# Optimization experiments

Hardware: AMD Instinct MI355X
Metric: run time of the kernel (lower is better)

The kernel has to match this reference:

```python
import jax, jax.numpy as jnp
import numpy as np

EMBED = 1024
HEADS = 16
HEAD_DIM = EMBED // HEADS


def setup_inputs() -> dict:
    key = jax.random.key(0)
    ks = jax.random.split(key, 8)
    N, S = 4, 2048
    scale = 1.0 / np.sqrt(HEAD_DIM)
    return {
        "values": jax.random.normal(ks[0], (N, S, EMBED), jnp.float32),
        "keys": jax.random.normal(ks[1], (N, S, EMBED), jnp.float32),
        "query": jax.random.normal(ks[2], (N, S, EMBED), jnp.float32),
        "Wv": jax.random.normal(ks[3], (HEAD_DIM, HEAD_DIM), jnp.float32) * scale,
        "Wk": jax.random.normal(ks[4], (HEAD_DIM, HEAD_DIM), jnp.float32) * scale,
        "Wq": jax.random.normal(ks[5], (HEAD_DIM, HEAD_DIM), jnp.float32) * scale,
        "Wo": jax.random.normal(ks[6], (EMBED, EMBED), jnp.float32) / np.sqrt(EMBED),
        "bo": jax.random.normal(ks[7], (EMBED,), jnp.float32) * 0.01,
    }


def reference(values, keys, query, Wv, Wk, Wq, Wo, bo):
    N = query.shape[0]
    # reshape to [N, S, H, D]
    v = values.reshape(N, -1, HEADS, HEAD_DIM)
    k = keys.reshape(N, -1, HEADS, HEAD_DIM)
    q = query.reshape(N, -1, HEADS, HEAD_DIM)
    # per-head linear projections (torch Linear: x @ W.T)
    v = jnp.einsum("nshd,ed->nshe", v, Wv)
    k = jnp.einsum("nshd,ed->nshe", k, Wk)
    q = jnp.einsum("nshd,ed->nshe", q, Wq)
    # full attention matrix [N, H, Q, K]; note scale uses embed_size**0.5 as in source
    energy = jnp.einsum("nqhd,nkhd->nhqk", q, k)
    attn = jax.nn.softmax(energy / jnp.sqrt(jnp.asarray(EMBED, energy.dtype)), axis=3)
    out = jnp.einsum("nhql,nlhd->nqhd", attn, v).reshape(N, -1, EMBED)
    return out @ Wo.T + bo
```

## Files before the change

### kernel.cpp

```cpp
#include <hip/hip_runtime.h>
#include <hip/hip_bf16.h>

#define EMBED 1024
#define HEADS 16
#define HD    64
#define NB    4
#define SEQ   2048

typedef __bf16 bf16x2 __attribute__((ext_vector_type(2)));
typedef __bf16 bf16x8 __attribute__((ext_vector_type(8)));
typedef float  f32x4  __attribute__((ext_vector_type(4)));
typedef float  f32x16 __attribute__((ext_vector_type(16)));
typedef unsigned uint2v __attribute__((ext_vector_type(2)));

__device__ __forceinline__ unsigned short f2bf(float f) {
    union { float f; unsigned u; } v; v.f = f;
    unsigned r = v.u + 0x7fffu + ((v.u >> 16) & 1u);
    return (unsigned short)(r >> 16);
}
__device__ __forceinline__ unsigned pack2(float a, float b) {
#if __has_builtin(__builtin_amdgcn_cvt_pk_bf16_f32)
    union { bf16x2 v; unsigned u; } c;
    c.v = __builtin_amdgcn_cvt_pk_bf16_f32(a, b);
    return c.u;
#else
    return (unsigned)f2bf(a) | ((unsigned)f2bf(b) << 16);
#endif
}

__global__ __launch_bounds__(256) void cvt_kernel(const float* __restrict__ src,
                                                  unsigned* __restrict__ dst) {
    int i = blockIdx.x * 256 + threadIdx.x;
    float4 v = ((const float4*)src)[i];
    uint2 o;
    o.x = pack2(v.x, v.y);
    o.y = pack2(v.z, v.w);
    ((uint2*)dst)[i] = o;
}

__global__ __launch_bounds__(256) void proj_kernel(
    const float* __restrict__ xq, const float* __restrict__ xk, const float* __restrict__ xv,
    const float* __restrict__ Wq, const float* __restrict__ Wk, const float* __restrict__ Wv,
    unsigned short* __restrict__ Qp, unsigned short* __restrict__ Kp, unsigned short* __restrict__ Vt)
{
    __shared__ __align__(16) unsigned short Wl[64 * 72];
    __shared__ __align__(16) unsigned short Xl[256 * 72];

    int bx = blockIdx.x;
    int p  = bx >> 9;
    int r  = bx & 511;
    int st = r & 7, h = (r >> 3) & 15, n = r >> 7;
    int s0 = st * 256;

    const float* x = (p == 0) ? xq : (p == 1) ? xk : xv;
    const float* W = (p == 0) ? Wq : (p == 1) ? Wk : Wv;
    const float sc = (p == 0) ? 0.045084220027780106f : 1.0f;

    int tid = threadIdx.x;

    for (int i = 0; i < 4; ++i) {
        int idx = tid + i * 256;
        int row = idx >> 4, c4 = idx & 15;
        float4 wv = ((const float4*)W)[row * 16 + c4];
        uint2 pw;
        pw.x = pack2(wv.x, wv.y);
        pw.y = pack2(wv.z, wv.w);
        *(uint2*)&Wl[row * 72 + c4 * 4] = pw;
    }
    const float* xbase = x + (size_t)(n * SEQ + s0) * EMBED + h * HD;
    for (int i = 0; i < 16; ++i) {
        int idx = tid + i * 256;
        int row = idx >> 4, c4 = idx & 15;
        float4 v = *(const float4*)(xbase + (size_t)row * EMBED + c4 * 4);
        uint2 px;
        px.x = pack2(v.x, v.y);
        px.y = pack2(v.z, v.w);
        *(uint2*)&Xl[row * 72 + c4 * 4] = px;
    }
    __syncthreads();

    int w = tid >> 6, lane = tid & 63, ln = lane & 15, qd = lane >> 4;

    bf16x8 a[4][2], b[4][2];
#pragma unroll
    for (int mt = 0; mt < 4; ++mt)
#pragma unroll
        for (int kt = 0; kt < 2; ++kt)
            a[mt][kt] = *(const bf16x8*)&Xl[(w * 64 + mt * 16 + ln) * 72 + kt * 32 + qd * 8];
#pragma unroll
    for (int i = 0; i < 4; ++i)
#pragma unroll
        for (int kt = 0; kt < 2; ++kt)
            b[i][kt] = *(const bf16x8*)&Wl[(i * 16 + ln) * 72 + kt * 32 + qd * 8];

    f32x4 acc[4][4];
    const f32x4 fz = {0.f, 0.f, 0.f, 0.f};
#pragma unroll
    for (int i = 0; i < 4; ++i)
#pragma unroll
        for (int j = 0; j < 4; ++j) acc[i][j] = fz;

    if (p < 2) {
#pragma unroll
        for (int i = 0; i < 4; ++i)
#pragma unroll
            for (int j = 0; j < 4; ++j) {
                acc[i][j] = __builtin_amdgcn_mfma_f32_16x16x32_bf16(b[i][0], a[j][0], acc[i][j], 0, 0, 0);
                acc[i][j] = __builtin_amdgcn_mfma_f32_16x16x32_bf16(b[i][1], a[j][1], acc[i][j], 0, 0, 0);
            }
#pragma unroll
        for (int i = 0; i < 4; ++i)
#pragma unroll
            for (int j = 0; j < 4; ++j) {
                uint2 pk;
                pk.x = pack2(acc[i][j][0] * sc, acc[i][j][1] * sc);
                pk.y = pack2(acc[i][j][2] * sc, acc[i][j][3] * sc);
                *(uint2*)&Xl[(w * 64 + j * 16 + ln) * 72 + i * 16 + qd * 4] = pk;
            }
        __syncthreads();
        unsigned short* outp = (p == 0 ? Qp : Kp) + (size_t)(n * HEADS + h) * SEQ * HD + (size_t)s0 * HD;
        for (int i = 0; i < 8; ++i) {
            int idx = tid + i * 256;
            int row = idx >> 3, ch = idx & 7;
            *(uint4*)(outp + (size_t)row * HD + ch * 8) = *(const uint4*)&Xl[row * 72 + ch * 8];
        }
    } else {
#pragma unroll
        for (int mt = 0; mt < 4; ++mt)
#pragma unroll
            for (int i = 0; i < 4; ++i) {
                acc[mt][i] = __builtin_amdgcn_mfma_f32_16x16x32_bf16(a[mt][0], b[i][0], acc[mt][i], 0, 0, 0);
                acc[mt][i] = __builtin_amdgcn_mfma_f32_16x16x32_bf16(a[mt][1], b[i][1], acc[mt][i], 0, 0, 0);
            }
        __syncthreads();
#pragma unroll
        for (int mt = 0; mt < 4; ++mt)
#pragma unroll
            for (int i = 0; i < 4; ++i) {
                uint2 pk;
                pk.x = pack2(acc[mt][i][0], acc[mt][i][1]);
                pk.y = pack2(acc[mt][i][2], acc[mt][i][3]);
                *(uint2*)&Xl[(i * 16 + ln) * 264 + w * 64 + mt * 16 + qd * 4] = pk;
            }
        __syncthreads();
        unsigned short* outp = Vt + (size_t)(n * HEADS + h) * HD * SEQ + s0;
        for (int i = 0; i < 8; ++i) {
            int idx = tid + i * 256;
            int row = idx >> 5, ch = idx & 31;
            *(uint4*)(outp + (size_t)row * SEQ + ch * 8) = *(const uint4*)&Xl[row * 264 + ch * 8];
        }
    }
}

__global__ __launch_bounds__(512, 4) void attn_kernel(
    const unsigned short* __restrict__ Qp, const unsigned short* __restrict__ Kp,
    const unsigned short* __restrict__ Vt, unsigned short* __restrict__ Xattn)
{
    __shared__ __align__(16) unsigned short SMEM[18432];
    unsigned short* Kl = SMEM;
    unsigned short* Vl = SMEM + 9216;

    int bx = blockIdx.x;
    int head = bx >> 3, qt = bx & 7;
    int n = head >> 4, h16 = head & 15;
    int q0 = qt * 256;

    int tid = threadIdx.x;
    int w = tid >> 6, lane = tid & 63;
    int qc = lane & 31, hh = lane >> 5;

    const unsigned short* Qb = Qp + (size_t)head * SEQ * HD;
    const unsigned short* Kb = Kp + (size_t)head * SEQ * HD;
    const unsigned short* Vb = Vt + (size_t)head * HD * SEQ;

    bf16x8 qb[4];
    {
        int qrow = q0 + w * 32 + qc;
#pragma unroll
        for (int kk = 0; kk < 4; ++kk)
            qb[kk] = *(const bf16x8*)(Qb + (size_t)qrow * HD + kk * 16 + hh * 8);
    }

    f32x16 ot0, ot1;
#pragma unroll
    for (int i = 0; i < 16; ++i) { ot0[i] = 0.f; ot1[i] = 0.f; }
    float ls[4] = {0.f, 0.f, 0.f, 0.f};

    int srow = tid >> 3, sch = tid & 7;

    uint4 rK, rV;
    rK = *(const uint4*)(Kb + (size_t)srow * HD + sch * 8);
    rV = *(const uint4*)(Vb + (size_t)srow * SEQ + 0 + sch * 8);
    *(uint4*)&Kl[srow * 72 + sch * 8] = rK;
    *(uint4*)&Vl[srow * 72 + sch * 8] = rV;
    rK = *(const uint4*)(Kb + (size_t)(64 + srow) * HD + sch * 8);
    rV = *(const uint4*)(Vb + (size_t)srow * SEQ + 64 + sch * 8);

    for (int kc = 0; kc < SEQ; kc += 64) {
        int cur = (kc >> 6) & 1, nxt = cur ^ 1;
        int curo = cur * 4608;
        __syncthreads();

        if (kc + 64 < SEQ) {
            *(uint4*)&Kl[nxt * 4608 + srow * 72 + sch * 8] = rK;
            *(uint4*)&Vl[nxt * 4608 + srow * 72 + sch * 8] = rV;
            int kn = kc + 128 <= SEQ - 64 ? kc + 128 : SEQ - 64;
            rK = *(const uint4*)(Kb + (size_t)(kn + srow) * HD + sch * 8);
            rV = *(const uint4*)(Vb + (size_t)srow * SEQ + kn + sch * 8);
        }

        unsigned pk[2][8];
#pragma unroll
        for (int kt = 0; kt < 2; ++kt) {
            f32x16 c;
#pragma unroll
            for (int i = 0; i < 16; ++i) c[i] = 0.f;
#pragma unroll
            for (int kk = 0; kk < 4; ++kk) {
                bf16x8 ka = *(const bf16x8*)&Kl[curo + (kt * 32 + qc) * 72 + kk * 16 + hh * 8];
                c = __builtin_amdgcn_mfma_f32_32x32x16_bf16(ka, qb[kk], c, 0, 0, 0);
            }
#pragma unroll
            for (int i = 0; i < 8; ++i) {
                float p0 = __builtin_amdgcn_exp2f(c[2 * i]);
                float p1 = __builtin_amdgcn_exp2f(c[2 * i + 1]);
                ls[i & 3] += p0 + p1;
                pk[kt][i] = pack2(p0, p1);
            }
        }

#pragma unroll
        for (int g = 0; g < 4; ++g) {
            const unsigned* P = pk[g >> 1];
            int base = (g & 1) * 4;
            union { unsigned u[4]; bf16x8 v; } bb;
#if __has_builtin(__builtin_amdgcn_permlane32_swap)
            uint2v r  = __builtin_amdgcn_permlane32_swap(P[base + 0], P[base + 2], false, false);
            uint2v rr = __builtin_amdgcn_permlane32_swap(P[base + 1], P[base + 3], false, false);
            bb.u[0] = r.x;
            bb.u[1] = rr.x;
            bb.u[2] = r.y;
            bb.u[3] = rr.y;
#else
            unsigned s0 = hh ? P[base + 0] : P[base + 2];
            unsigned s1 = hh ? P[base + 1] : P[base + 3];
            unsigned r0 = (unsigned)__shfl_xor((int)s0, 32);
            unsigned r1 = (unsigned)__shfl_xor((int)s1, 32);
            bb.u[0] = hh ? r0 : P[base + 0];
            bb.u[1] = hh ? r1 : P[base + 1];
            bb.u[2] = hh ? P[base + 2] : r0;
            bb.u[3] = hh ? P[base + 3] : r1;
#endif
            bf16x8 va0 = *(const bf16x8*)&Vl[curo + qc * 72 + g * 16 + hh * 8];
            bf16x8 va1 = *(const bf16x8*)&Vl[curo + (32 + qc) * 72 + g * 16 + hh * 8];
            ot0 = __builtin_amdgcn_mfma_f32_32x32x16_bf16(va0, bb.v, ot0, 0, 0, 0);
            ot1 = __builtin_amdgcn_mfma_f32_32x32x16_bf16(va1, bb.v, ot1, 0, 0, 0);
        }
    }

    float lsum = (ls[0] + ls[1]) + (ls[2] + ls[3]);
    lsum += __shfl_xor(lsum, 32);
    float inv = 1.0f / lsum;

    __syncthreads();
    int qlocal = w * 32 + qc;
#pragma unroll
    for (int dt = 0; dt < 2; ++dt) {
        const f32x16& o = dt ? ot1 : ot0;
#pragma unroll
        for (int g = 0; g < 4; ++g) {
            uint2 p;
            p.x = pack2(o[4 * g + 0] * inv, o[4 * g + 1] * inv);
            p.y = pack2(o[4 * g + 2] * inv, o[4 * g + 3] * inv);
            *(uint2*)&SMEM[qlocal * 72 + dt * 32 + g * 8 + hh * 4] = p;
        }
    }
    __syncthreads();
    unsigned short* ob = Xattn + (size_t)(n * SEQ + q0) * EMBED + h16 * HD;
#pragma unroll
    for (int i = 0; i < 4; ++i) {
        int idx = tid + i * 512;
        int row = idx >> 3, ch = idx & 7;
        *(uint4*)(ob + (size_t)row * EMBED + ch * 8) = *(const uint4*)&SMEM[row * 72 + ch * 8];
    }
}

__global__ __launch_bounds__(256, 4) void outproj_kernel(
    const unsigned short* __restrict__ X, const unsigned short* __restrict__ Wb,
    const float* __restrict__ bo, float* __restrict__ out)
{
    __shared__ __align__(16) unsigned short Al[64 * 72];
    __shared__ __align__(16) unsigned short Bl[128 * 72];

    int bx = blockIdx.x;
    int cm = bx >> 3, cn = bx & 7;
    int m0 = cm * 64, c0 = cn * 128;
    int tid = threadIdx.x;
    int w = tid >> 6, lane = tid & 63, ln = lane & 15, qd = lane >> 4;
    int chw = w * 32;

    f32x4 acc[4][2];
    const f32x4 fz = {0.f, 0.f, 0.f, 0.f};
#pragma unroll
    for (int mt = 0; mt < 4; ++mt)
#pragma unroll
        for (int nt = 0; nt < 2; ++nt) acc[mt][nt] = fz;

    for (int k0 = 0; k0 < EMBED; k0 += 64) {
        {
            int row = tid >> 3, ch = tid & 7;
            if (tid < 512) {
            }
#pragma unroll
            for (int i = 0; i < 2; ++i) {
                int idx = tid + i * 256;
                int r2 = idx >> 3, c2 = idx & 7;
                uint4 av = *(const uint4*)(X + (size_t)(m0 + r2) * EMBED + k0 + c2 * 8);
                *(uint4*)&Al[r2 * 72 + c2 * 8] = av;
            }
#pragma unroll
            for (int i = 0; i < 4; ++i) {
                int idx = tid + i * 256;
                int r2 = idx >> 3, c2 = idx & 7;
                uint4 bv = *(const uint4*)(Wb + (size_t)(c0 + r2) * EMBED + k0 + c2 * 8);
                *(uint4*)&Bl[r2 * 72 + c2 * 8] = bv;
            }
            (void)row; (void)ch;
        }
        __syncthreads();
        bf16x8 af[4][2], bf_[2][2];
#pragma unroll
        for (int mt = 0; mt < 4; ++mt)
#pragma unroll
            for (int kt = 0; kt < 2; ++kt)
                af[mt][kt] = *(const bf16x8*)&Al[(mt * 16 + ln) * 72 + kt * 32 + qd * 8];
#pragma unroll
        for (int nt = 0; nt < 2; ++nt)
#pragma unroll
            for (int kt = 0; kt < 2; ++kt)
                bf_[nt][kt] = *(const bf16x8*)&Bl[(chw + nt * 16 + ln) * 72 + kt * 32 + qd * 8];
#pragma unroll
        for (int mt = 0; mt < 4; ++mt)
#pragma unroll
            for (int nt = 0; nt < 2; ++nt) {
                acc[mt][nt] = __builtin_amdgcn_mfma_f32_16x16x32_bf16(af[mt][0], bf_[nt][0], acc[mt][nt], 0, 0, 0);
                acc[mt][nt] = __builtin_amdgcn_mfma_f32_16x16x32_bf16(af[mt][1], bf_[nt][1], acc[mt][nt], 0, 0, 0);
            }
        __syncthreads();
    }

#pragma unroll
    for (int nt = 0; nt < 2; ++nt) {
        int col = c0 + chw + nt * 16 + ln;
        float bias = bo[col];
#pragma unroll
        for (int mt = 0; mt < 4; ++mt) {
            int row = m0 + mt * 16 + qd * 4;
#pragma unroll
            for (int rg = 0; rg < 4; ++rg)
                out[(size_t)(row + rg) * EMBED + col] = acc[mt][nt][rg] + bias;
        }
    }
}

extern "C" void kernel_launch(void* const* d_in, const int* in_sizes, int n_in,
                              void* d_out, int out_size, void* d_ws, size_t ws_size,
                              hipStream_t stream) {
    const float* values = (const float*)d_in[0];
    const float* keys   = (const float*)d_in[1];
    const float* query  = (const float*)d_in[2];
    const float* Wv     = (const float*)d_in[3];
    const float* Wk     = (const float*)d_in[4];
    const float* Wq     = (const float*)d_in[5];
    const float* Wo     = (const float*)d_in[6];
    const float* bo     = (const float*)d_in[7];
    float* out = (float*)d_out;

    unsigned short* ws = (unsigned short*)d_ws;
    const size_t HSZ = (size_t)NB * HEADS * SEQ * HD;
    unsigned short* Qp = ws;
    unsigned short* Kp = Qp + HSZ;
    unsigned short* Vt = Kp + HSZ;
    unsigned short* Xa = Vt + HSZ;
    unsigned short* Wb = Xa + HSZ;

    cvt_kernel<<<1024, 256, 0, stream>>>(Wo, (unsigned*)Wb);
    proj_kernel<<<1536, 256, 0, stream>>>(query, keys, values, Wq, Wk, Wv, Qp, Kp, Vt);
    attn_kernel<<<512, 512, 0, stream>>>(Qp, Kp, Vt, Xa);
    outproj_kernel<<<1024, 256, 0, stream>>>(Xa, Wb, bo, out);
}
```

Baseline: 271.8 us.

## Split attention into 128-query blocks, swizzle block order, add MFMA priority hints

The attention kernel moves from 512-thread blocks covering 256 queries to 256-thread blocks covering 128 queries, doubling the grid to 1024 blocks. Each thread now stages two K/V rows per tile. Blocks are remapped so consecutive block IDs spread across heads (likely for XCD/L2 locality), and s_setprio raises wave priority around the MFMA sections. The smaller blocks aim for better occupancy and load balance, but each K/V tile is now loaded twice as often per query.

After: 334.0 us. +22.9%, slower.

```diff
diff --git a/kernel.cpp b/kernel.cpp
--- a/kernel.cpp
+++ b/kernel.cpp
@@ -152,7 +152,7 @@
     }
 }
 
-__global__ __launch_bounds__(512, 4) void attn_kernel(
+__global__ __launch_bounds__(256, 4) void attn_kernel(
     const unsigned short* __restrict__ Qp, const unsigned short* __restrict__ Kp,
     const unsigned short* __restrict__ Vt, unsigned short* __restrict__ Xattn)
 {
@@ -160,10 +160,11 @@
     unsigned short* Kl = SMEM;
     unsigned short* Vl = SMEM + 9216;
 
-    int bx = blockIdx.x;
-    int head = bx >> 3, qt = bx & 7;
+    int pb = blockIdx.x;
+    int bx = (pb & 7) * 128 + (pb >> 3);
+    int head = bx >> 4, qt = bx & 15;
     int n = head >> 4, h16 = head & 15;
-    int q0 = qt * 256;
+    int q0 = qt * 128;
 
     int tid = threadIdx.x;
     int w = tid >> 6, lane = tid & 63;
@@ -188,13 +189,21 @@
 
     int srow = tid >> 3, sch = tid & 7;
 
-    uint4 rK, rV;
-    rK = *(const uint4*)(Kb + (size_t)srow * HD + sch * 8);
-    rV = *(const uint4*)(Vb + (size_t)srow * SEQ + 0 + sch * 8);
-    *(uint4*)&Kl[srow * 72 + sch * 8] = rK;
-    *(uint4*)&Vl[srow * 72 + sch * 8] = rV;
-    rK = *(const uint4*)(Kb + (size_t)(64 + srow) * HD + sch * 8);
-    rV = *(const uint4*)(Vb + (size_t)srow * SEQ + 64 + sch * 8);
+    uint4 rK[2], rV[2];
+#pragma unroll
+    for (int i = 0; i < 2; ++i) {
+        int rr = srow + i * 32;
+        rK[i] = *(const uint4*)(Kb + (size_t)rr * HD + sch * 8);
+        rV[i] = *(const uint4*)(Vb + (size_t)rr * SEQ + 0 + sch * 8);
+        *(uint4*)&Kl[rr * 72 + sch * 8] = rK[i];
+        *(uint4*)&Vl[rr * 72 + sch * 8] = rV[i];
+    }
+#pragma unroll
+    for (int i = 0; i < 2; ++i) {
+        int rr = srow + i * 32;
+        rK[i] = *(const uint4*)(Kb + (size_t)(64 + rr) * HD + sch * 8);
+        rV[i] = *(const uint4*)(Vb + (size_t)rr * SEQ + 64 + sch * 8);
+    }
 
     for (int kc = 0; kc < SEQ; kc += 64) {
         int cur = (kc >> 6) & 1, nxt = cur ^ 1;
@@ -202,11 +211,19 @@
         __syncthreads();
 
         if (kc + 64 < SEQ) {
-            *(uint4*)&Kl[nxt * 4608 + srow * 72 + sch * 8] = rK;
-            *(uint4*)&Vl[nxt * 4608 + srow * 72 + sch * 8] = rV;
+#pragma unroll
+            for (int i = 0; i < 2; ++i) {
+                int rr = srow + i * 32;
+                *(uint4*)&Kl[nxt * 4608 + rr * 72 + sch * 8] = rK[i];
+                *(uint4*)&Vl[nxt * 4608 + rr * 72 + sch * 8] = rV[i];
+            }
             int kn = kc + 128 <= SEQ - 64 ? kc + 128 : SEQ - 64;
-            rK = *(const uint4*)(Kb + (size_t)(kn + srow) * HD + sch * 8);
-            rV = *(const uint4*)(Vb + (size_t)srow * SEQ + kn + sch * 8);
+#pragma unroll
+            for (int i = 0; i < 2; ++i) {
+                int rr = srow + i * 32;
+                rK[i] = *(const uint4*)(Kb + (size_t)(kn + rr) * HD + sch * 8);
+                rV[i] = *(const uint4*)(Vb + (size_t)rr * SEQ + kn + sch * 8);
+            }
         }
 
         unsigned pk[2][8];
@@ -215,11 +232,13 @@
             f32x16 c;
 #pragma unroll
             for (int i = 0; i < 16; ++i) c[i] = 0.f;
+            __builtin_amdgcn_s_setprio(1);
 #pragma unroll
             for (int kk = 0; kk < 4; ++kk) {
                 bf16x8 ka = *(const bf16x8*)&Kl[curo + (kt * 32 + qc) * 72 + kk * 16 + hh * 8];
                 c = __builtin_amdgcn_mfma_f32_32x32x16_bf16(ka, qb[kk], c, 0, 0, 0);
             }
+            __builtin_amdgcn_s_setprio(0);
 #pragma unroll
             for (int i = 0; i < 8; ++i) {
                 float p0 = __builtin_amdgcn_exp2f(c[2 * i]);
@@ -229,6 +248,7 @@
             }
         }
 
+        __builtin_amdgcn_s_setprio(1);
 #pragma unroll
         for (int g = 0; g < 4; ++g) {
             const unsigned* P = pk[g >> 1];
@@ -256,6 +276,7 @@
             ot0 = __builtin_amdgcn_mfma_f32_32x32x16_bf16(va0, bb.v, ot0, 0, 0, 0);
             ot1 = __builtin_amdgcn_mfma_f32_32x32x16_bf16(va1, bb.v, ot1, 0, 0, 0);
         }
+        __builtin_amdgcn_s_setprio(0);
     }
 
     float lsum = (ls[0] + ls[1]) + (ls[2] + ls[3]);
@@ -279,7 +300,7 @@
     unsigned short* ob = Xattn + (size_t)(n * SEQ + q0) * EMBED + h16 * HD;
 #pragma unroll
     for (int i = 0; i < 4; ++i) {
-        int idx = tid + i * 512;
+        int idx = tid + i * 256;
         int row = idx >> 3, ch = idx & 7;
         *(uint4*)(ob + (size_t)row * EMBED + ch * 8) = *(const uint4*)&SMEM[row * 72 + ch * 8];
     }
@@ -308,9 +329,6 @@
 
     for (int k0 = 0; k0 < EMBED; k0 += 64) {
         {
-            int row = tid >> 3, ch = tid & 7;
-            if (tid < 512) {
-            }
 #pragma unroll
             for (int i = 0; i < 2; ++i) {
                 int idx = tid + i * 256;
@@ -325,7 +343,6 @@
                 uint4 bv = *(const uint4*)(Wb + (size_t)(c0 + r2) * EMBED + k0 + c2 * 8);
                 *(uint4*)&Bl[r2 * 72 + c2 * 8] = bv;
             }
-            (void)row; (void)ch;
         }
         __syncthreads();
         bf16x8 af[4][2], bf_[2][2];
@@ -386,6 +403,6 @@
 
     cvt_kernel<<<1024, 256, 0, stream>>>(Wo, (unsigned*)Wb);
     proj_kernel<<<1536, 256, 0, stream>>>(query, keys, values, Wq, Wk, Wv, Qp, Kp, Vt);
-    attn_kernel<<<512, 512, 0, stream>>>(Qp, Kp, Vt, Xa);
+    attn_kernel<<<1024, 256, 0, stream>>>(Qp, Kp, Vt, Xa);
     outproj_kernel<<<1024, 256, 0, stream>>>(Xa, Wb, bo, out);
 }
```

## Fuse all four stages into one persistent kernel with grid barriers

Applied to the files above, without the earlier changes.

Merges the Wo conversion, QKV projection, attention and output projection into a single 512-block persistent kernel. The stages are separated by a software grid barrier, an atomic counter plus a generation flag stored in the last two words of the output buffer and zeroed by a memset. This removes the launch gaps and tail effects between separate kernels. The projection now runs three smaller tiles per block, and the output projection moves to 128x128 tiles on 512 blocks. The design relies on all blocks being co-resident, and the barrier words are later overwritten by output writes. A spin timeout can silently break synchronisation.

Measured after the change: 451.6 us. +66.1%, slower.

```diff
diff --git a/kernel.cpp b/kernel.cpp
--- a/kernel.cpp
+++ b/kernel.cpp
@@ -6,6 +6,7 @@
 #define HD    64
 #define NB    4
 #define SEQ   2048
+#define NBLK  512
 
 typedef __bf16 bf16x2 __attribute__((ext_vector_type(2)));
 typedef __bf16 bf16x8 __attribute__((ext_vector_type(8)));
@@ -28,337 +29,352 @@
 #endif
 }
 
-__global__ __launch_bounds__(256) void cvt_kernel(const float* __restrict__ src,
-                                                  unsigned* __restrict__ dst) {
-    int i = blockIdx.x * 256 + threadIdx.x;
-    float4 v = ((const float4*)src)[i];
-    uint2 o;
-    o.x = pack2(v.x, v.y);
-    o.y = pack2(v.z, v.w);
-    ((uint2*)dst)[i] = o;
-}
-
-__global__ __launch_bounds__(256) void proj_kernel(
-    const float* __restrict__ xq, const float* __restrict__ xk, const float* __restrict__ xv,
-    const float* __restrict__ Wq, const float* __restrict__ Wk, const float* __restrict__ Wv,
-    unsigned short* __restrict__ Qp, unsigned short* __restrict__ Kp, unsigned short* __restrict__ Vt)
-{
-    __shared__ __align__(16) unsigned short Wl[64 * 72];
-    __shared__ __align__(16) unsigned short Xl[256 * 72];
-
-    int bx = blockIdx.x;
-    int p  = bx >> 9;
-    int r  = bx & 511;
-    int st = r & 7, h = (r >> 3) & 15, n = r >> 7;
-    int s0 = st * 256;
-
-    const float* x = (p == 0) ? xq : (p == 1) ? xk : xv;
-    const float* W = (p == 0) ? Wq : (p == 1) ? Wk : Wv;
-    const float sc = (p == 0) ? 0.045084220027780106f : 1.0f;
-
-    int tid = threadIdx.x;
-
-    for (int i = 0; i < 4; ++i) {
-        int idx = tid + i * 256;
-        int row = idx >> 4, c4 = idx & 15;
-        float4 wv = ((const float4*)W)[row * 16 + c4];
-        uint2 pw;
-        pw.x = pack2(wv.x, wv.y);
-        pw.y = pack2(wv.z, wv.w);
-        *(uint2*)&Wl[row * 72 + c4 * 4] = pw;
-    }
-    const float* xbase = x + (size_t)(n * SEQ + s0) * EMBED + h * HD;
-    for (int i = 0; i < 16; ++i) {
-        int idx = tid + i * 256;
-        int row = idx >> 4, c4 = idx & 15;
-        float4 v = *(const float4*)(xbase + (size_t)row * EMBED + c4 * 4);
-        uint2 px;
-        px.x = pack2(v.x, v.y);
-        px.y = pack2(v.z, v.w);
-        *(uint2*)&Xl[row * 72 + c4 * 4] = px;
+__device__ __forceinline__ void grid_barrier(unsigned* cnt, unsigned* gen, unsigned phase) {
+    __syncthreads();
+    if (threadIdx.x == 0) {
+        __threadfence();
+        unsigned prev = atomicAdd(cnt, 1u);
+        if (prev == NBLK * (phase + 1) - 1) {
+            __hip_atomic_store(gen, phase + 1, __ATOMIC_RELEASE, __HIP_MEMORY_SCOPE_AGENT);
+        } else {
+            long long spins = 0;
+            while (__hip_atomic_load(gen, __ATOMIC_ACQUIRE, __HIP_MEMORY_SCOPE_AGENT) < phase + 1) {
+                __builtin_amdgcn_s_sleep(2);
+                if (++spins > (1LL << 22)) break;
+            }
+        }
+        __threadfence();
     }
     __syncthreads();
-
-    int w = tid >> 6, lane = tid & 63, ln = lane & 15, qd = lane >> 4;
-
-    bf16x8 a[4][2], b[4][2];
-#pragma unroll
-    for (int mt = 0; mt < 4; ++mt)
-#pragma unroll
-        for (int kt = 0; kt < 2; ++kt)
-            a[mt][kt] = *(const bf16x8*)&Xl[(w * 64 + mt * 16 + ln) * 72 + kt * 32 + qd * 8];
-#pragma unroll
-    for (int i = 0; i < 4; ++i)
-#pragma unroll
-        for (int kt = 0; kt < 2; ++kt)
-            b[i][kt] = *(const bf16x8*)&Wl[(i * 16 + ln) * 72 + kt * 32 + qd * 8];
-
-    f32x4 acc[4][4];
-    const f32x4 fz = {0.f, 0.f, 0.f, 0.f};
-#pragma unroll
-    for (int i = 0; i < 4; ++i)
-#pragma unroll
-        for (int j = 0; j < 4; ++j) acc[i][j] = fz;
-
-    if (p < 2) {
-#pragma unroll
-        for (int i = 0; i < 4; ++i)
-#pragma unroll
-            for (int j = 0; j < 4; ++j) {
-                acc[i][j] = __builtin_amdgcn_mfma_f32_16x16x32_bf16(b[i][0], a[j][0], acc[i][j], 0, 0, 0);
-                acc[i][j] = __builtin_amdgcn_mfma_f32_16x16x32_bf16(b[i][1], a[j][1], acc[i][j], 0, 0, 0);
-            }
-#pragma unroll
-        for (int i = 0; i < 4; ++i)
-#pragma unroll
-            for (int j = 0; j < 4; ++j) {
-                uint2 pk;
-                pk.x = pack2(acc[i][j][0] * sc, acc[i][j][1] * sc);
-                pk.y = pack2(acc[i][j][2] * sc, acc[i][j][3] * sc);
-                *(uint2*)&Xl[(w * 64 + j * 16 + ln) * 72 + i * 16 + qd * 4] = pk;
-            }
+}
+
+__global__ __launch_bounds__(512, 4) void mega_kernel(
+    const float* __restrict__ values, const float* __restrict__ keys,
+    const float* __restrict__ query,
+    const float* __restrict__ Wv, const float* __restrict__ Wk,
+    const float* __restrict__ Wq,
+    const float* __restrict__ Wo, const float* __restrict__ bo,
+    unsigned short* __restrict__ Qp, unsigned short* __restrict__ Kp,
+    unsigned short* __restrict__ Vt, unsigned short* __restrict__ Xa,
+    unsigned short* __restrict__ Wb, float* __restrict__ out)
+{
+    __shared__ __align__(16) unsigned short SMEM[23040];
+    unsigned* bar = (unsigned*)(out + (size_t)NB * SEQ * EMBED - 2);
+
+    int bx = blockIdx.x;
+    int tid = threadIdx.x;
+
+    {
+        int i = bx * 512 + tid;
+        float4 v = ((const float4*)Wo)[i];
+        uint2 o;
+        o.x = pack2(v.x, v.y);
+        o.y = pack2(v.z, v.w);
+        ((uint2*)Wb)[i] = o;
+    }
+
+    {
+        unsigned short* Wl = SMEM;
+        unsigned short* Xl = SMEM + 4608;
+        int w = tid >> 6, lane = tid & 63, ln = lane & 15, qd = lane >> 4;
+
+        for (int t = 0; t < 3; ++t) {
+            int id = bx * 3 + t;
+            int p = id >> 9, r = id & 511;
+            int st = r & 7, h = (r >> 3) & 15, n = r >> 7;
+            int s0 = st * 256;
+            const float* x = (p == 0) ? query : (p == 1) ? keys : values;
+            const float* W = (p == 0) ? Wq : (p == 1) ? Wk : Wv;
+            const float sc = (p == 0) ? 0.045084220027780106f : 1.0f;
+
+            __syncthreads();
+#pragma unroll
+            for (int i2 = 0; i2 < 2; ++i2) {
+                int idx = tid + i2 * 512;
+                int row = idx >> 4, c4 = idx & 15;
+                float4 wv = ((const float4*)W)[row * 16 + c4];
+                uint2 pw;
+                pw.x = pack2(wv.x, wv.y);
+                pw.y = pack2(wv.z, wv.w);
+                *(uint2*)&Wl[row * 72 + c4 * 4] = pw;
+            }
+            const float* xbase = x + (size_t)(n * SEQ + s0) * EMBED + h * HD;
+#pragma unroll
+            for (int i2 = 0; i2 < 8; ++i2) {
+                int idx = tid + i2 * 512;
+                int row = idx >> 4, c4 = idx & 15;
+                float4 v = *(const float4*)(xbase + (size_t)row * EMBED + c4 * 4);
+                uint2 px;
+                px.x = pack2(v.x, v.y);
+                px.y = pack2(v.z, v.w);
+                *(uint2*)&Xl[row * 72 + c4 * 4] = px;
+            }
+            __syncthreads();
+
+            bf16x8 a[2][2], b[4][2];
+#pragma unroll
+            for (int mt = 0; mt < 2; ++mt)
+#pragma unroll
+                for (int kt = 0; kt < 2; ++kt)
+                    a[mt][kt] = *(const bf16x8*)&Xl[(w * 32 + mt * 16 + ln) * 72 + kt * 32 + qd * 8];
+#pragma unroll
+            for (int i2 = 0; i2 < 4; ++i2)
+#pragma unroll
+                for (int kt = 0; kt < 2; ++kt)
+                    b[i2][kt] = *(const bf16x8*)&Wl[(i2 * 16 + ln) * 72 + kt * 32 + qd * 8];
+
+            f32x4 acc[4][2];
+            const f32x4 fz = {0.f, 0.f, 0.f, 0.f};
+#pragma unroll
+            for (int i2 = 0; i2 < 4; ++i2)
+#pragma unroll
+                for (int j = 0; j < 2; ++j) acc[i2][j] = fz;
+
+            if (p < 2) {
+#pragma unroll
+                for (int i2 = 0; i2 < 4; ++i2)
+#pragma unroll
+                    for (int j = 0; j < 2; ++j) {
+                        acc[i2][j] = __builtin_amdgcn_mfma_f32_16x16x32_bf16(b[i2][0], a[j][0], acc[i2][j], 0, 0, 0);
+                        acc[i2][j] = __builtin_amdgcn_mfma_f32_16x16x32_bf16(b[i2][1], a[j][1], acc[i2][j], 0, 0, 0);
+                    }
+#pragma unroll
+                for (int i2 = 0; i2 < 4; ++i2)
+#pragma unroll
+                    for (int j = 0; j < 2; ++j) {
+                        uint2 pk;
+                        pk.x = pack2(acc[i2][j][0] * sc, acc[i2][j][1] * sc);
+                        pk.y = pack2(acc[i2][j][2] * sc, acc[i2][j][3] * sc);
+                        *(uint2*)&Xl[(w * 32 + j * 16 + ln) * 72 + i2 * 16 + qd * 4] = pk;
+                    }
+                __syncthreads();
+                unsigned short* outp = (p == 0 ? Qp : Kp) + (size_t)(n * HEADS + h) * SEQ * HD + (size_t)s0 * HD;
+#pragma unroll
+                for (int i2 = 0; i2 < 4; ++i2) {
+                    int idx = tid + i2 * 512;
+                    int row = idx >> 3, ch = idx & 7;
+                    *(uint4*)(outp + (size_t)row * HD + ch * 8) = *(const uint4*)&Xl[row * 72 + ch * 8];
+                }
+            } else {
+#pragma unroll
+                for (int mt = 0; mt < 2; ++mt)
+#pragma unroll
+                    for (int i2 = 0; i2 < 4; ++i2) {
+                        acc[i2][mt] = __builtin_amdgcn_mfma_f32_16x16x32_bf16(a[mt][0], b[i2][0], acc[i2][mt], 0, 0, 0);
+                        acc[i2][mt] = __builtin_amdgcn_mfma_f32_16x16x32_bf16(a[mt][1], b[i2][1], acc[i2][mt], 0, 0, 0);
+                    }
+                __syncthreads();
+#pragma unroll
+                for (int mt = 0; mt < 2; ++mt)
+#pragma unroll
+                    for (int i2 = 0; i2 < 4; ++i2) {
+                        uint2 pk;
+                        pk.x = pack2(acc[i2][mt][0], acc[i2][mt][1]);
+                        pk.y = pack2(acc[i2][mt][2], acc[i2][mt][3]);
+                        *(uint2*)&Xl[(i2 * 16 + ln) * 264 + w * 32 + mt * 16 + qd * 4] = pk;
+                    }
+                __syncthreads();
+                unsigned short* outp = Vt + (size_t)(n * HEADS + h) * HD * SEQ + s0;
+#pragma unroll
+                for (int i2 = 0; i2 < 4; ++i2) {
+                    int idx = tid + i2 * 512;
+                    int row = idx >> 5, ch = idx & 31;
+                    *(uint4*)(outp + (size_t)row * SEQ + ch * 8) = *(const uint4*)&Xl[row * 264 + ch * 8];
+                }
+            }
+        }
+    }
+
+    grid_barrier(bar, bar + 1, 0);
+
+    {
+        unsigned short* Kl = SMEM;
+        unsigned short* Vl = SMEM + 9216;
+
+        int head = bx >> 3, qt = bx & 7;
+        int n = head >> 4, h16 = head & 15;
+        int q0 = qt * 256;
+
+        int w = tid >> 6, lane = tid & 63;
+        int qc = lane & 31, hh = lane >> 5;
+
+        const unsigned short* Qb = Qp + (size_t)head * SEQ * HD;
+        const unsigned short* Kb = Kp + (size_t)head * SEQ * HD;
+        const unsigned short* Vb = Vt + (size_t)head * HD * SEQ;
+
+        bf16x8 qb[4];
+        {
+            int qrow = q0 + w * 32 + qc;
+#pragma unroll
+            for (int kk = 0; kk < 4; ++kk)
+                qb[kk] = *(const bf16x8*)(Qb + (size_t)qrow * HD + kk * 16 + hh * 8);
+        }
+
+        f32x16 ot0, ot1;
+#pragma unroll
+        for (int i = 0; i < 16; ++i) { ot0[i] = 0.f; ot1[i] = 0.f; }
+        float ls[4] = {0.f, 0.f, 0.f, 0.f};
+
+        int srow = tid >> 3, sch = tid & 7;
+
+        uint4 rK, rV;
+        rK = *(const uint4*)(Kb + (size_t)srow * HD + sch * 8);
+        rV = *(const uint4*)(Vb + (size_t)srow * SEQ + 0 + sch * 8);
+        *(uint4*)&Kl[srow * 72 + sch * 8] = rK;
+        *(uint4*)&Vl[srow * 72 + sch * 8] = rV;
+        rK = *(const uint4*)(Kb + (size_t)(64 + srow) * HD + sch * 8);
+        rV = *(const uint4*)(Vb + (size_t)srow * SEQ + 64 + sch * 8);
+
+        for (int kc = 0; kc < SEQ; kc += 64) {
+            int cur = (kc >> 6) & 1, nxt = cur ^ 1;
+            int curo = cur * 4608;
+            __syncthreads();
+
+            if (kc + 64 < SEQ) {
+                *(uint4*)&Kl[nxt * 4608 + srow * 72 + sch * 8] = rK;
+                *(uint4*)&Vl[nxt * 4608 + srow * 72 + sch * 8] = rV;
+                int kn = kc + 128 <= SEQ - 64 ? kc + 128 : SEQ - 64;
+                rK = *(const uint4*)(Kb + (size_t)(kn + srow) * HD + sch * 8);
+                rV = *(const uint4*)(Vb + (size_t)srow * SEQ + kn + sch * 8);
+            }
+
+            unsigned pk[2][8];
+#pragma unroll
+            for (int kt = 0; kt < 2; ++kt) {
+                f32x16 c;
+#pragma unroll
+                for (int i = 0; i < 16; ++i) c[i] = 0.f;
+#pragma unroll
+                for (int kk = 0; kk < 4; ++kk) {
+                    bf16x8 ka = *(const bf16x8*)&Kl[curo + (kt * 32 + qc) * 72 + kk * 16 + hh * 8];
+                    c = __builtin_amdgcn_mfma_f32_32x32x16_bf16(ka, qb[kk], c, 0, 0, 0);
+                }
+#pragma unroll
+                for (int i = 0; i < 8; ++i) {
+                    float p0 = __builtin_amdgcn_exp2f(c[2 * i]);
+                    float p1 = __builtin_amdgcn_exp2f(c[2 * i + 1]);
+                    ls[i & 3] += p0 + p1;
+                    pk[kt][i] = pack2(p0, p1);
+                }
+            }
+
+#pragma unroll
+            for (int g = 0; g < 4; ++g) {
+                const unsigned* P = pk[g >> 1];
+                int base = (g & 1) * 4;
+                union { unsigned u[4]; bf16x8 v; } bb;
+#if __has_builtin(__builtin_amdgcn_permlane32_swap)
+                uint2v rr0 = __builtin_amdgcn_permlane32_swap(P[base + 0], P[base + 2], false, false);
+                uint2v rr1 = __builtin_amdgcn_permlane32_swap(P[base + 1], P[base + 3], false, false);
+                bb.u[0] = rr0.x;
+                bb.u[1] = rr1.x;
+                bb.u[2] = rr0.y;
+                bb.u[3] = rr1.y;
+#else
+                unsigned s0_ = hh ? P[base + 0] : P[base + 2];
+                unsigned s1_ = hh ? P[base + 1] : P[base + 3];
+                unsigned r0_ = (unsigned)__shfl_xor((int)s0_, 32);
+                unsigned r1_ = (unsigned)__shfl_xor((int)s1_, 32);
+                bb.u[0] = hh ? r0_ : P[base + 0];
+                bb.u[1] = hh ? r1_ : P[base + 1];
+                bb.u[2] = hh ? P[base + 2] : r0_;
+                bb.u[3] = hh ? P[base + 3] : r1_;
+#endif
+                bf16x8 va0 = *(const bf16x8*)&Vl[curo + qc * 72 + g * 16 + hh * 8];
+                bf16x8 va1 = *(const bf16x8*)&Vl[curo + (32 + qc) * 72 + g * 16 + hh * 8];
+                ot0 = __builtin_amdgcn_mfma_f32_32x32x16_bf16(va0, bb.v, ot0, 0, 0, 0);
+                ot1 = __builtin_amdgcn_mfma_f32_32x32x16_bf16(va1, bb.v, ot1, 0, 0, 0);
+            }
+        }
+
+        float lsum = (ls[0] + ls[1]) + (ls[2] + ls[3]);
+        lsum += __shfl_xor(lsum, 32);
+        float inv = 1.0f / lsum;
+
         __syncthreads();
-        unsigned short* outp = (p == 0 ? Qp : Kp) + (size_t)(n * HEADS + h) * SEQ * HD + (size_t)s0 * HD;
-        for (int i = 0; i < 8; ++i) {
-            int idx = tid + i * 256;
+        int qlocal = w * 32 + qc;
+#pragma unroll
+        for (int dt = 0; dt < 2; ++dt) {
+            const f32x16& o = dt ? ot1 : ot0;
+#pragma unroll
+            for (int g = 0; g < 4; ++g) {
+                uint2 p;
+                p.x = pack2(o[4 * g + 0] * inv, o[4 * g + 1] * inv);
+                p.y = pack2(o[4 * g + 2] * inv, o[4 * g + 3] * inv);
+                *(uint2*)&SMEM[qlocal * 72 + dt * 32 + g * 8 + hh * 4] = p;
+            }
+        }
+        __syncthreads();
+        unsigned short* ob = Xa + (size_t)(n * SEQ + q0) * EMBED + h16 * HD;
+#pragma unroll
+        for (int i = 0; i < 4; ++i) {
+            int idx = tid + i * 512;
             int row = idx >> 3, ch = idx & 7;
-            *(uint4*)(outp + (size_t)row * HD + ch * 8) = *(const uint4*)&Xl[row * 72 + ch * 8];
-        }
-    } else {
+            *(uint4*)(ob + (size_t)row * EMBED + ch * 8) = *(const uint4*)&SMEM[row * 72 + ch * 8];
+        }
+    }
+
+    grid_barrier(bar, bar + 1, 1);
+
+    {
+        unsigned short* Al = SMEM;
+        unsigned short* Bl = SMEM + 9216;
+
+        int cm = bx >> 3, cn = bx & 7;
+        int m0 = cm * 128, c0 = cn * 128;
+        int w = tid >> 6, lane = tid & 63, ln = lane & 15, qd = lane >> 4;
+        int wr = w >> 2, wc = w & 3;
+
+        int r1 = tid >> 3, ch = tid & 7;
+        const unsigned short* Xb = Xa + (size_t)(m0 + r1) * EMBED + ch * 8;
+        const unsigned short* Wbb = Wb + (size_t)(c0 + r1) * EMBED + ch * 8;
+
+        f32x4 acc[4][2];
+        const f32x4 fz = {0.f, 0.f, 0.f, 0.f};
 #pragma unroll
         for (int mt = 0; mt < 4; ++mt)
 #pragma unroll
-            for (int i = 0; i < 4; ++i) {
-                acc[mt][i] = __builtin_amdgcn_mfma_f32_16x16x32_bf16(a[mt][0], b[i][0], acc[mt][i], 0, 0, 0);
-                acc[mt][i] = __builtin_amdgcn_mfma_f32_16x16x32_bf16(a[mt][1], b[i][1], acc[mt][i], 0, 0, 0);
-            }
-        __syncthreads();
-#pragma unroll
-        for (int mt = 0; mt < 4; ++mt)
-#pragma unroll
-            for (int i = 0; i < 4; ++i) {
-                uint2 pk;
-                pk.x = pack2(acc[mt][i][0], acc[mt][i][1]);
-                pk.y = pack2(acc[mt][i][2], acc[mt][i][3]);
-                *(uint2*)&Xl[(i * 16 + ln) * 264 + w * 64 + mt * 16 + qd * 4] = pk;
-            }
-        __syncthreads();
-        unsigned short* outp = Vt + (size_t)(n * HEADS + h) * HD * SEQ + s0;
-        for (int i = 0; i < 8; ++i) {
-            int idx = tid + i * 256;
-            int row = idx >> 5, ch = idx & 31;
-            *(uint4*)(outp + (size_t)row * SEQ + ch * 8) = *(const uint4*)&Xl[row * 264 + ch * 8];
-        }
-    }
-}
-
-__global__ __launch_bounds__(512, 4) void attn_kernel(
-    const unsigned short* __restrict__ Qp, const unsigned short* __restrict__ Kp,
-    const unsigned short* __restrict__ Vt, unsigned short* __restrict__ Xattn)
-{
-    __shared__ __align__(16) unsigned short SMEM[18432];
-    unsigned short* Kl = SMEM;
-    unsigned short* Vl = SMEM + 9216;
-
-    int bx = blockIdx.x;
-    int head = bx >> 3, qt = bx & 7;
-    int n = head >> 4, h16 = head & 15;
-    int q0 = qt * 256;
-
-    int tid = threadIdx.x;
-    int w = tid >> 6, lane = tid & 63;
-    int qc = lane & 31, hh = lane >> 5;
-
-    const unsigned short* Qb = Qp + (size_t)head * SEQ * HD;
-    const unsigned short* Kb = Kp + (size_t)head * SEQ * HD;
-    const unsigned short* Vb = Vt + (size_t)head * HD * SEQ;
-
-    bf16x8 qb[4];
-    {
-        int qrow = q0 + w * 32 + qc;
-#pragma unroll
-        for (int kk = 0; kk < 4; ++kk)
-            qb[kk] = *(const bf16x8*)(Qb + (size_t)qrow * HD + kk * 16 + hh * 8);
-    }
-
-    f32x16 ot0, ot1;
-#pragma unroll
-    for (int i = 0; i < 16; ++i) { ot0[i] = 0.f; ot1[i] = 0.f; }
-    float ls[4] = {0.f, 0.f, 0.f, 0.f};
-
-    int srow = tid >> 3, sch = tid & 7;
-
-    uint4 rK, rV;
-    rK = *(const uint4*)(Kb + (size_t)srow * HD + sch * 8);
-    rV = *(const uint4*)(Vb + (size_t)srow * SEQ + 0 + sch * 8);
-    *(uint4*)&Kl[srow * 72 + sch * 8] = rK;
-    *(uint4*)&Vl[srow * 72 + sch * 8] = rV;
-    rK = *(const uint4*)(Kb + (size_t)(64 + srow) * HD + sch * 8);
-    rV = *(const uint4*)(Vb + (size_t)srow * SEQ + 64 + sch * 8);
-
-    for (int kc = 0; kc < SEQ; kc += 64) {
-        int cur = (kc >> 6) & 1, nxt = cur ^ 1;
-        int curo = cur * 4608;
-        __syncthreads();
-
-        if (kc + 64 < SEQ) {
-            *(uint4*)&Kl[nxt * 4608 + srow * 72 + sch * 8] = rK;
-            *(uint4*)&Vl[nxt * 4608 + srow * 72 + sch * 8] = rV;
-            int kn = kc + 128 <= SEQ - 64 ? kc + 128 : SEQ - 64;
-            rK = *(const uint4*)(Kb + (size_t)(kn + srow) * HD + sch * 8);
-            rV = *(const uint4*)(Vb + (size_t)srow * SEQ + kn + sch * 8);
-        }
-
-        unsigned pk[2][8];
-#pragma unroll
-        for (int kt = 0; kt < 2; ++kt) {
-            f32x16 c;
-#pragma unroll
-            for (int i = 0; i < 16; ++i) c[i] = 0.f;
-#pragma unroll
-            for (int kk = 0; kk < 4; ++kk) {
-                bf16x8 ka = *(const bf16x8*)&Kl[curo + (kt * 32 + qc) * 72 + kk * 16 + hh * 8];
-                c = __builtin_amdgcn_mfma_f32_32x32x16_bf16(ka, qb[kk], c, 0, 0, 0);
-            }
-#pragma unroll
-            for (int i = 0; i < 8; ++i) {
-                float p0 = __builtin_amdgcn_exp2f(c[2 * i]);
-                float p1 = __builtin_amdgcn_exp2f(c[2 * i + 1]);
-                ls[i & 3] += p0 + p1;
-                pk[kt][i] = pack2(p0, p1);
-            }
-        }
-
-#pragma unroll
-        for (int g = 0; g < 4; ++g) {
-            const unsigned* P = pk[g >> 1];
-            int base = (g & 1) * 4;
-            union { unsigned u[4]; bf16x8 v; } bb;
-#if __has_builtin(__builtin_amdgcn_permlane32_swap)
-            uint2v r  = __builtin_amdgcn_permlane32_swap(P[base + 0], P[base + 2], false, false);
-            uint2v rr = __builtin_amdgcn_permlane32_swap(P[base + 1], P[base + 3], false, false);
-            bb.u[0] = r.x;
-            bb.u[1] = rr.x;
-            bb.u[2] = r.y;
-            bb.u[3] = rr.y;
-#else
-            unsigned s0 = hh ? P[base + 0] : P[base + 2];
-            unsigned s1 = hh ? P[base + 1] : P[base + 3];
-            unsigned r0 = (unsigned)__shfl_xor((int)s0, 32);
-            unsigned r1 = (unsigned)__shfl_xor((int)s1, 32);
-            bb.u[0] = hh ? r0 : P[base + 0];
-            bb.u[1] = hh ? r1 : P[base + 1];
-            bb.u[2] = hh ? P[base + 2] : r0;
-            bb.u[3] = hh ? P[base + 3] : r1;
-#endif
-            bf16x8 va0 = *(const bf16x8*)&Vl[curo + qc * 72 + g * 16 + hh * 8];
-            bf16x8 va1 = *(const bf16x8*)&Vl[curo + (32 + qc) * 72 + g * 16 + hh * 8];
-            ot0 = __builtin_amdgcn_mfma_f32_32x32x16_bf16(va0, bb.v, ot0, 0, 0, 0);
-            ot1 = __builtin_amdgcn_mfma_f32_32x32x16_bf16(va1, bb.v, ot1, 0, 0, 0);
-        }
-    }
-
-    float lsum = (ls[0] + ls[1]) + (ls[2] + ls[3]);
-    lsum += __shfl_xor(lsum, 32);
-    float inv = 1.0f / lsum;
-
-    __syncthreads();
-    int qlocal = w * 32 + qc;
-#pragma unroll
-    for (int dt = 0; dt < 2; ++dt) {
-        const f32x16& o = dt ? ot1 : ot0;
-#pragma unroll
-        for (int g = 0; g < 4; ++g) {
-            uint2 p;
-            p.x = pack2(o[4 * g + 0] * inv, o[4 * g + 1] * inv);
-            p.y = pack2(o[4 * g + 2] * inv, o[4 * g + 3] * inv);
-            *(uint2*)&SMEM[qlocal * 72 + dt * 32 + g * 8 + hh * 4] = p;
-        }
-    }
-    __syncthreads();
-    unsigned short* ob = Xattn + (size_t)(n * SEQ + q0) * EMBED + h16 * HD;
-#pragma unroll
-    for (int i = 0; i < 4; ++i) {
-        int idx = tid + i * 512;
-        int row = idx >> 3, ch = idx & 7;
-        *(uint4*)(ob + (size_t)row * EMBED + ch * 8) = *(const uint4*)&SMEM[row * 72 + ch * 8];
-    }
-}
-
-__global__ __launch_bounds__(256, 4) void outproj_kernel(
-    const unsigned short* __restrict__ X, const unsigned short* __restrict__ Wb,
-    const float* __restrict__ bo, float* __restrict__ out)
-{
-    __shared__ __align__(16) unsigned short Al[64 * 72];
-    __shared__ __align__(16) unsigned short Bl[128 * 72];
-
-    int bx = blockIdx.x;
-    int cm = bx >> 3, cn = bx & 7;
-    int m0 = cm * 64, c0 = cn * 128;
-    int tid = threadIdx.x;
-    int w = tid >> 6, lane = tid & 63, ln = lane & 15, qd = lane >> 4;
-    int chw = w * 32;
-
-    f32x4 acc[4][2];
-    const f32x4 fz = {0.f, 0.f, 0.f, 0.f};
-#pragma unroll
-    for (int mt = 0; mt < 4; ++mt)
-#pragma unroll
-        for (int nt = 0; nt < 2; ++nt) acc[mt][nt] = fz;
-
-    for (int k0 = 0; k0 < EMBED; k0 += 64) {
-        {
-            int row = tid >> 3, ch = tid & 7;
-            if (tid < 512) {
-            }
-#pragma unroll
-            for (int i = 0; i < 2; ++i) {
-                int idx = tid + i * 256;
-                int r2 = idx >> 3, c2 = idx & 7;
-                uint4 av = *(const uint4*)(X + (size_t)(m0 + r2) * EMBED + k0 + c2 * 8);
-                *(uint4*)&Al[r2 * 72 + c2 * 8] = av;
-            }
-#pragma unroll
-            for (int i = 0; i < 4; ++i) {
-                int idx = tid + i * 256;
-                int r2 = idx >> 3, c2 = idx & 7;
-                uint4 bv = *(const uint4*)(Wb + (size_t)(c0 + r2) * EMBED + k0 + c2 * 8);
-                *(uint4*)&Bl[r2 * 72 + c2 * 8] = bv;
-            }
-            (void)row; (void)ch;
-        }
-        __syncthreads();
-        bf16x8 af[4][2], bf_[2][2];
-#pragma unroll
-        for (int mt = 0; mt < 4; ++mt)
-#pragma unroll
-            for (int kt = 0; kt < 2; ++kt)
-                af[mt][kt] = *(const bf16x8*)&Al[(mt * 16 + ln) * 72 + kt * 32 + qd * 8];
-#pragma unroll
-        for (int nt = 0; nt < 2; ++nt)
-#pragma unroll
-            for (int kt = 0; kt < 2; ++kt)
-                bf_[nt][kt] = *(const bf16x8*)&Bl[(chw + nt * 16 + ln) * 72 + kt * 32 + qd * 8];
-#pragma unroll
-        for (int mt = 0; mt < 4; ++mt)
-#pragma unroll
-            for (int nt = 0; nt < 2; ++nt) {
-                acc[mt][nt] = __builtin_amdgcn_mfma_f32_16x16x32_bf16(af[mt][0], bf_[nt][0], acc[mt][nt], 0, 0, 0);
-                acc[mt][nt] = __builtin_amdgcn_mfma_f32_16x16x32_bf16(af[mt][1], bf_[nt][1], acc[mt][nt], 0, 0, 0);
-            }
-        __syncthreads();
-    }
-
-#pragma unroll
-    for (int nt = 0; nt < 2; ++nt) {
-        int col = c0 + chw + nt * 16 + ln;
-        float bias = bo[col];
-#pragma unroll
-        for (int mt = 0; mt < 4; ++mt) {
-            int row = m0 + mt * 16 + qd * 4;
-#pragma unroll
-            for (int rg = 0; rg < 4; ++rg)
-                out[(size_t)(row + rg) * EMBED + col] = acc[mt][nt][rg] + bias;
+            for (int nt = 0; nt < 2; ++nt) acc[mt][nt] = fz;
+
+        for (int k0 = 0; k0 < EMBED; k0 += 64) {
+            __syncthreads();
+            *(uint4*)&Al[r1 * 72 + ch * 8]        = *(const uint4*)(Xb + k0);
+            *(uint4*)&Al[(r1 + 64) * 72 + ch * 8] = *(const uint4*)(Xb + (size_t)64 * EMBED + k0);
+            *(uint4*)&Bl[r1 * 72 + ch * 8]        = *(const uint4*)(Wbb + k0);
+            *(uint4*)&Bl[(r1 + 64) * 72 + ch * 8] = *(const uint4*)(Wbb + (size_t)64 * EMBED + k0);
+            __syncthreads();
+
+            bf16x8 af[4][2], bf_[2][2];
+#pragma unroll
+            for (int mt = 0; mt < 4; ++mt)
+#pragma unroll
+                for (int kt = 0; kt < 2; ++kt)
+                    af[mt][kt] = *(const bf16x8*)&Al[(wr * 64 + mt * 16 + ln) * 72 + kt * 32 + qd * 8];
+#pragma unroll
+            for (int nt = 0; nt < 2; ++nt)
+#pragma unroll
+                for (int kt = 0; kt < 2; ++kt)
+                    bf_[nt][kt] = *(const bf16x8*)&Bl[(wc * 32 + nt * 16 + ln) * 72 + kt * 32 + qd * 8];
+#pragma unroll
+            for (int mt = 0; mt < 4; ++mt)
+#pragma unroll
+                for (int nt = 0; nt < 2; ++nt) {
+                    acc[mt][nt] = __builtin_amdgcn_mfma_f32_16x16x32_bf16(af[mt][0], bf_[nt][0], acc[mt][nt], 0, 0, 0);
+                    acc[mt][nt] = __builtin_amdgcn_mfma_f32_16x16x32_bf16(af[mt][1], bf_[nt][1], acc[mt][nt], 0, 0, 0);
+                }
+        }
+
+#pragma unroll
+        for (int nt = 0; nt < 2; ++nt) {
+            int col = c0 + wc * 32 + nt * 16 + ln;
+            float bias = bo[col];
+#pragma unroll
+            for (int mt = 0; mt < 4; ++mt) {
+                int row = m0 + wr * 64 + mt * 16 + qd * 4;
+#pragma unroll
+                for (int rg = 0; rg < 4; ++rg)
+                    out[(size_t)(row + rg) * EMBED + col] = acc[mt][nt][rg] + bias;
+            }
         }
     }
 }
@@ -384,8 +400,7 @@
     unsigned short* Xa = Vt + HSZ;
     unsigned short* Wb = Xa + HSZ;
 
-    cvt_kernel<<<1024, 256, 0, stream>>>(Wo, (unsigned*)Wb);
-    proj_kernel<<<1536, 256, 0, stream>>>(query, keys, values, Wq, Wk, Wv, Qp, Kp, Vt);
-    attn_kernel<<<512, 512, 0, stream>>>(Qp, Kp, Vt, Xa);
-    outproj_kernel<<<1024, 256, 0, stream>>>(Xa, Wb, bo, out);
+    hipMemsetAsync(out + (size_t)NB * SEQ * EMBED - 2, 0, 8, stream);
+    mega_kernel<<<NBLK, 512, 0, stream>>>(values, keys, query, Wv, Wk, Wq, Wo, bo,
+                                          Qp, Kp, Vt, Xa, Wb, out);
 }
```
